# Kernel optimization log

Measured on AMD Instinct MI355X. Metric: run time of the kernel, lower is better.

## Reference

```python
import jax, jax.numpy as jnp
import numpy as np

N, E = 50000, 1600000
D_IN, H, N_REL, D_OUT = 518, 256, 10, 128


def setup_inputs() -> dict:
    key = jax.random.key(0)
    ks = jax.random.split(key, 20)
    def lin(k, fan_in, fan_out):
        bound = 1.0 / np.sqrt(fan_in)
        kw, kb = jax.random.split(k)
        W = jax.random.uniform(kw, (fan_in, fan_out), jnp.float32, -bound, bound)
        b = jax.random.uniform(kb, (fan_out,), jnp.float32, -bound, bound)
        return W, b
    x = jax.random.normal(ks[0], (N, D_IN), jnp.float32)
    edge_index = jax.random.randint(ks[1], (2, E), 0, N, jnp.int32)
    edge_attr = jax.random.randint(ks[2], (E,), 0, N_REL, jnp.int32)
    W_enc1, b_enc1 = lin(ks[3], D_IN, H)
    W_enc2, b_enc2 = lin(ks[4], H, H)
    emb_table = jax.random.normal(ks[5], (N_REL, H // 4), jnp.float32)
    W_g1, b_g1 = lin(ks[6], H, H)
    W_g2, b_g2 = lin(ks[7], H, H)
    W_g3, b_g3 = lin(ks[8], H, H)
    W_h1, b_h1 = lin(ks[9], H, H // 2)
    W_h2, b_h2 = lin(ks[10], H // 2, D_OUT)
    return dict(x=x, edge_index=edge_index, edge_attr=edge_attr,
                W_enc1=W_enc1, b_enc1=b_enc1, W_enc2=W_enc2, b_enc2=b_enc2,
                emb_table=emb_table,
                W_g1=W_g1, b_g1=b_g1, W_g2=W_g2, b_g2=b_g2, W_g3=W_g3, b_g3=b_g3,
                W_h1=W_h1, b_h1=b_h1, W_h2=W_h2, b_h2=b_h2)


def reference(x, edge_index, edge_attr,
              W_enc1, b_enc1, W_enc2, b_enc2, emb_table,
              W_g1, b_g1, W_g2, b_g2, W_g3, b_g3,
              W_h1, b_h1, W_h2, b_h2):
    src, dst = edge_index[0], edge_index[1]
    n = x.shape[0]
    # GCN symmetric normalization with self-loops: deg = 1 + in-degree
    deg = 1.0 + jax.ops.segment_sum(jnp.ones_like(src, jnp.float32), dst, num_segments=n)
    dis = deg ** -0.5                       # [N]
    norm_e = dis[src] * dis[dst]            # [E] edge norm
    self_norm = (dis * dis)[:, None]        # [N,1] self-loop norm

    def gcn(h, W, b):
        hw = h @ W                           # [N,H]
        agg = jax.ops.segment_sum(hw[src] * norm_e[:, None], dst, num_segments=n)
        return agg + hw * self_norm + b

    # node encoder (dropout is identity in eval)
    h = jax.nn.relu(x @ W_enc1 + b_enc1) @ W_enc2 + b_enc2
    _edge_emb = emb_table[edge_attr]         # computed as in original (unused downstream)
    h = jax.nn.relu(gcn(h, W_g1, b_g1))
    h = jax.nn.relu(gcn(h, W_g2, b_g2))
    h = jax.nn.relu(gcn(h, W_g3, b_g3))
    graph_repr = jnp.mean(h, axis=0, keepdims=True)   # batch=None path -> [1,H]
    out = jax.nn.relu(graph_repr @ W_h1 + b_h1) @ W_h2 + b_h2
    return out
```

## Files before the change

### kernel.cpp

```cpp
#include <hip/hip_runtime.h>

#define D_IN 518
#define HD 256
#define KP1 544
#define AGG_CAP 4096

typedef __attribute__((ext_vector_type(8))) short bf16x8;
typedef __attribute__((ext_vector_type(4))) float f32x4;
typedef __attribute__((ext_vector_type(4), aligned(4))) float float4u;
typedef __attribute__((ext_vector_type(4))) unsigned int uint4v;
typedef __attribute__((ext_vector_type(8))) unsigned short ushort8v;

__device__ __forceinline__ float bf2f(unsigned short u) {
  union { unsigned int i; float f; } v; v.i = ((unsigned int)u) << 16; return v.f;
}
__device__ __forceinline__ unsigned short f2bf(float f) {
  union { float f; unsigned int i; } v; v.f = f;
  unsigned int r = (v.i + 0x7FFFu + ((v.i >> 16) & 1u)) >> 16;
  return (unsigned short)r;
}

__global__ void k_canary(float* __restrict__ out, float code) {
  out[threadIdx.x] = code;
}


__global__ void k_hist(const int* __restrict__ dst, int E, int* __restrict__ cnt) {
  int e = (blockIdx.x * blockDim.x + threadIdx.x) * 4;
  if (e < E) {
    int4 d = *(const int4*)(dst + e);
    atomicAdd(&cnt[d.x], 1);
    atomicAdd(&cnt[d.y], 1);
    atomicAdd(&cnt[d.z], 1);
    atomicAdd(&cnt[d.w], 1);
  }
}

__global__ void k_blocksum(const int* __restrict__ cnt, int n, int* __restrict__ bsum) {
  __shared__ int red[256];
  const int t = threadIdx.x;
  int v = blockIdx.x * 256 + t;
  red[t] = (v < n) ? cnt[v] : 0;
  __syncthreads();
  for (int d = 128; d > 0; d >>= 1) {
    if (t < d) red[t] += red[t + d];
    __syncthreads();
  }
  if (t == 0) bsum[blockIdx.x] = red[0];
}

__global__ void k_scan_mid(const int* __restrict__ bsum, int nb, int* __restrict__ bex) {
  __shared__ int s[256];
  const int t = threadIdx.x;
  int x = (t < nb) ? bsum[t] : 0;
  s[t] = x;
  __syncthreads();
  for (int d = 1; d < 256; d <<= 1) {
    int v = (t >= d) ? s[t - d] : 0;
    __syncthreads();
    s[t] += v;
    __syncthreads();
  }
  if (t < nb) bex[t] = s[t] - x;
}

__global__ void k_off(const int* __restrict__ cnt, int n, const int* __restrict__ bex,
                      int* __restrict__ off, int* __restrict__ cursor,
                      float* __restrict__ dis) {
  __shared__ int s[256];
  const int t = threadIdx.x;
  const int v = blockIdx.x * 256 + t;
  int c = (v < n) ? cnt[v] : 0;
  s[t] = c;
  __syncthreads();
  for (int d = 1; d < 256; d <<= 1) {
    int x = (t >= d) ? s[t - d] : 0;
    __syncthreads();
    s[t] += x;
    __syncthreads();
  }
  if (v < n) {
    int incl = bex[blockIdx.x] + s[t];
    off[v + 1] = incl;
    cursor[v] = incl - c;
    dis[v] = 1.0f / sqrtf(1.0f + (float)c);
    if (v == 0) off[0] = 0;
  }
}

__global__ void k_fill_range(const int* __restrict__ src, const int* __restrict__ dst, int E,
                             int* __restrict__ cursor, unsigned short* __restrict__ csr,
                             int lo, int hi) {
  int e = (blockIdx.x * blockDim.x + threadIdx.x) * 4;
  if (e < E) {
    int4 d = *(const int4*)(dst + e);
    int4 s = *(const int4*)(src + e);
    if (d.x >= lo && d.x < hi) csr[atomicAdd(&cursor[d.x], 1)] = (unsigned short)s.x;
    if (d.y >= lo && d.y < hi) csr[atomicAdd(&cursor[d.y], 1)] = (unsigned short)s.y;
    if (d.z >= lo && d.z < hi) csr[atomicAdd(&cursor[d.z], 1)] = (unsigned short)s.z;
    if (d.w >= lo && d.w < hi) csr[atomicAdd(&cursor[d.w], 1)] = (unsigned short)s.w;
  }
}


__global__ void k_wt(const float* __restrict__ W, int K, int N, int Kp,
                     unsigned short* __restrict__ Wt) {
  int idx = blockIdx.x * blockDim.x + threadIdx.x;
  if (idx < N * Kp) {
    int n = idx / Kp, k = idx - n * Kp;
    Wt[idx] = (k < K) ? f2bf(W[k * N + n]) : (unsigned short)0;
  }
}

__global__ void k_wt4(const float* __restrict__ a, const float* __restrict__ b,
                      const float* __restrict__ c, const float* __restrict__ d,
                      unsigned short* __restrict__ oa, unsigned short* __restrict__ ob,
                      unsigned short* __restrict__ oc, unsigned short* __restrict__ od) {
  const float* W = (blockIdx.y == 0) ? a : (blockIdx.y == 1) ? b : (blockIdx.y == 2) ? c : d;
  unsigned short* O = (blockIdx.y == 0) ? oa : (blockIdx.y == 1) ? ob : (blockIdx.y == 2) ? oc : od;
  int idx = blockIdx.x * blockDim.x + threadIdx.x;
  int n = idx >> 8, k = idx & 255;
  O[idx] = f2bf(W[k * HD + n]);
}


__global__ __launch_bounds__(256, 2)
void k_gemm_bt(const unsigned short* __restrict__ A, int lda, int M, int K,
               const unsigned short* __restrict__ Bt, int ldb,
               const float* __restrict__ bias, const float* __restrict__ rowscale,
               int do_relu,
               unsigned short* __restrict__ C, int ldc, int sliced, int Mp) {
  const int bid = blockIdx.x;
  const int pair = (bid >> 4) * 8 + (bid & 7);
  const int mtiles = (M + 127) >> 7;
  if (pair >= mtiles) return;
  const int m0 = pair << 7;
  const int n0 = ((bid >> 3) & 1) << 7;

  __shared__ unsigned short As[128 * 40];
  __shared__ unsigned short Bs[128 * 40];
  const int tid = threadIdx.x;
  const int lane = tid & 63, wave = tid >> 6;
  const int q = lane >> 4, l15 = lane & 15;
  const int wm = (wave & 1) * 64, wn = (wave >> 1) * 64;

  f32x4 acc[4][4];
#pragma unroll
  for (int i = 0; i < 4; i++)
#pragma unroll
    for (int j = 0; j < 4; j++) acc[i][j] = f32x4{0.f, 0.f, 0.f, 0.f};

  const int r0 = tid >> 2, kb = tid & 3;
  int gmA0 = m0 + r0;       if (gmA0 >= M) gmA0 = M - 1;
  int gmA1 = m0 + r0 + 64;  if (gmA1 >= M) gmA1 = M - 1;
  const unsigned short* Arow0 = A + (size_t)gmA0 * lda;
  const unsigned short* Arow1 = A + (size_t)gmA1 * lda;
  const unsigned short* Brow0 = Bt + (size_t)(n0 + r0) * ldb;
  const unsigned short* Brow1 = Bt + (size_t)(n0 + r0 + 64) * ldb;
  unsigned short* lA0 = &As[r0 * 40 + kb * 8];
  unsigned short* lA1 = &As[(r0 + 64) * 40 + kb * 8];
  unsigned short* lB0 = &Bs[r0 * 40 + kb * 8];
  unsigned short* lB1 = &Bs[(r0 + 64) * 40 + kb * 8];

  for (int k0 = 0; k0 < K; k0 += 32) {
    __syncthreads();
    const int gk = k0 + kb * 8;
    *(bf16x8*)lA0 = *(const bf16x8*)(Arow0 + gk);
    *(bf16x8*)lA1 = *(const bf16x8*)(Arow1 + gk);
    *(bf16x8*)lB0 = *(const bf16x8*)(Brow0 + gk);
    *(bf16x8*)lB1 = *(const bf16x8*)(Brow1 + gk);
    __syncthreads();

    bf16x8 af[4], bfr[4];
#pragma unroll
    for (int i = 0; i < 4; i++)
      af[i] = *(const bf16x8*)(&As[(wm + i * 16 + l15) * 40 + q * 8]);
#pragma unroll
    for (int j = 0; j < 4; j++)
      bfr[j] = *(const bf16x8*)(&Bs[(wn + j * 16 + l15) * 40 + q * 8]);
#pragma unroll
    for (int i = 0; i < 4; i++)
#pragma unroll
      for (int j = 0; j < 4; j++)
        acc[i][j] = __builtin_amdgcn_mfma_f32_16x16x32_bf16(af[i], bfr[j], acc[i][j], 0, 0, 0);
  }

  const size_t Mp32 = (size_t)Mp * 32;
#pragma unroll
  for (int j = 0; j < 4; j++) {
    const int col = n0 + wn + j * 16 + l15;
    const float bv = bias ? bias[col] : 0.f;
    unsigned short* cb = sliced ? (C + (size_t)(col >> 5) * Mp32 + (col & 31))
                                : (C + col);
    const int rstr = sliced ? 32 : ldc;
#pragma unroll
    for (int i = 0; i < 4; i++) {
#pragma unroll
      for (int rg = 0; rg < 4; rg++) {
        int gr = m0 + wm + i * 16 + q * 4 + rg;
        if (gr < M) {
          float v = acc[i][j][rg];
          if (rowscale) v *= rowscale[gr];
          v += bv;
          if (do_relu) v = fmaxf(v, 0.f);
          cb[(size_t)gr * rstr] = f2bf(v);
        }
      }
    }
  }
}


__global__ __launch_bounds__(256, 2)
void k_gemm_f32in(const float* __restrict__ A, int lda, int M, int Kreal, int Kloop,
                  const unsigned short* __restrict__ Bt, int ldb,
                  const float* __restrict__ bias, int do_relu,
                  unsigned short* __restrict__ C, int ldc) {
  const int bid = blockIdx.x;
  const int pair = (bid >> 4) * 8 + (bid & 7);
  const int mtiles = (M + 127) >> 7;
  if (pair >= mtiles) return;
  const int m0 = pair << 7;
  const int n0 = ((bid >> 3) & 1) << 7;

  __shared__ unsigned short As[128 * 40];
  __shared__ unsigned short Bs[128 * 40];
  const int tid = threadIdx.x;
  const int lane = tid & 63, wave = tid >> 6;
  const int q = lane >> 4, l15 = lane & 15;
  const int wm = (wave & 1) * 64, wn = (wave >> 1) * 64;

  f32x4 acc[4][4];
#pragma unroll
  for (int i = 0; i < 4; i++)
#pragma unroll
    for (int j = 0; j < 4; j++) acc[i][j] = f32x4{0.f, 0.f, 0.f, 0.f};

  const int r0 = tid >> 2, kb = tid & 3;
  int gmA0 = m0 + r0;       if (gmA0 >= M) gmA0 = M - 1;
  int gmA1 = m0 + r0 + 64;  if (gmA1 >= M) gmA1 = M - 1;
  const float* Arow0 = A + (size_t)gmA0 * lda;
  const float* Arow1 = A + (size_t)gmA1 * lda;
  const unsigned short* Brow0 = Bt + (size_t)(n0 + r0) * ldb;
  const unsigned short* Brow1 = Bt + (size_t)(n0 + r0 + 64) * ldb;
  unsigned short* lA0 = &As[r0 * 40 + kb * 8];
  unsigned short* lA1 = &As[(r0 + 64) * 40 + kb * 8];
  unsigned short* lB0 = &Bs[r0 * 40 + kb * 8];
  unsigned short* lB1 = &Bs[(r0 + 64) * 40 + kb * 8];

  for (int k0 = 0; k0 < Kloop; k0 += 32) {
    __syncthreads();
    const int gk = k0 + kb * 8;
    if (gk + 8 <= Kreal) {
      float4u a0 = *(const float4u*)(Arow0 + gk);
      float4u a1 = *(const float4u*)(Arow0 + gk + 4);
      float4u b0 = *(const float4u*)(Arow1 + gk);
      float4u b1 = *(const float4u*)(Arow1 + gk + 4);
      bf16x8 t0, t1;
      t0[0] = (short)f2bf(a0.x); t0[1] = (short)f2bf(a0.y);
      t0[2] = (short)f2bf(a0.z); t0[3] = (short)f2bf(a0.w);
      t0[4] = (short)f2bf(a1.x); t0[5] = (short)f2bf(a1.y);
      t0[6] = (short)f2bf(a1.z); t0[7] = (short)f2bf(a1.w);
      t1[0] = (short)f2bf(b0.x); t1[1] = (short)f2bf(b0.y);
      t1[2] = (short)f2bf(b0.z); t1[3] = (short)f2bf(b0.w);
      t1[4] = (short)f2bf(b1.x); t1[5] = (short)f2bf(b1.y);
      t1[6] = (short)f2bf(b1.z); t1[7] = (short)f2bf(b1.w);
      *(bf16x8*)lA0 = t0;
      *(bf16x8*)lA1 = t1;
    } else {
      bf16x8 t0, t1;
#pragma unroll
      for (int t = 0; t < 8; t++) {
        int kk = gk + t;
        t0[t] = (short)((kk < Kreal) ? f2bf(Arow0[kk]) : (unsigned short)0);
        t1[t] = (short)((kk < Kreal) ? f2bf(Arow1[kk]) : (unsigned short)0);
      }
      *(bf16x8*)lA0 = t0;
      *(bf16x8*)lA1 = t1;
    }
    *(bf16x8*)lB0 = *(const bf16x8*)(Brow0 + gk);
    *(bf16x8*)lB1 = *(const bf16x8*)(Brow1 + gk);
    __syncthreads();

    bf16x8 af[4], bfr[4];
#pragma unroll
    for (int i = 0; i < 4; i++)
      af[i] = *(const bf16x8*)(&As[(wm + i * 16 + l15) * 40 + q * 8]);
#pragma unroll
    for (int j = 0; j < 4; j++)
      bfr[j] = *(const bf16x8*)(&Bs[(wn + j * 16 + l15) * 40 + q * 8]);
#pragma unroll
    for (int i = 0; i < 4; i++)
#pragma unroll
      for (int j = 0; j < 4; j++)
        acc[i][j] = __builtin_amdgcn_mfma_f32_16x16x32_bf16(af[i], bfr[j], acc[i][j], 0, 0, 0);
  }

#pragma unroll
  for (int j = 0; j < 4; j++) {
    const int col = n0 + wn + j * 16 + l15;
    const float bv = bias ? bias[col] : 0.f;
#pragma unroll
    for (int i = 0; i < 4; i++) {
#pragma unroll
      for (int rg = 0; rg < 4; rg++) {
        int gr = m0 + wm + i * 16 + q * 4 + rg;
        if (gr < M) {
          float v = acc[i][j][rg] + bv;
          if (do_relu) v = fmaxf(v, 0.f);
          C[(size_t)gr * ldc + col] = f2bf(v);
        }
      }
    }
  }
}


__global__ __launch_bounds__(256, 6)
void k_agg_sl(const unsigned short* __restrict__ hw_sl, int Mp,
              const int* __restrict__ off, const unsigned short* __restrict__ csr,
              const float* __restrict__ dis, const float* __restrict__ bias,
              unsigned short* __restrict__ hout, int n) {
  __shared__ unsigned short lidx[AGG_CAP];
  __shared__ int lodd[65];
  const int slice = blockIdx.x & 7;
  const int chunk = blockIdx.x >> 3;
  const int tid = threadIdx.x;
  const int wave = tid >> 6, lane = tid & 63;
  const int eg = lane >> 2, cl = lane & 3;
  const unsigned short* panel = hw_sl + (size_t)slice * ((size_t)Mp * 32) + (cl << 3);

  const int base = chunk << 6;
  int nv = n - base; if (nv > 64) nv = 64;
  if (tid <= nv) lodd[tid] = off[base + tid];
  __syncthreads();
  const int blk_e0 = lodd[0];
  const int tot = lodd[nv] - blk_e0;
  const bool use_lds = (tot <= AGG_CAP);
  if (use_lds) {
    for (int i = tid; i < tot; i += 256) lidx[i] = csr[blk_e0 + i];
  }
  __syncthreads();

  const int lv = (wave << 4) + eg;
  if (lv >= nv) return;
  const int v = base + lv;
  const int e0 = lodd[lv];
  const int cnt = lodd[lv + 1] - e0;
  float a[8];
#pragma unroll
  for (int k = 0; k < 8; ++k) a[k] = 0.f;

  if (use_lds) {
    const int le = e0 - blk_e0;
    int it = 0;
    for (; it + 8 <= cnt; it += 8) {
      int s[8];
#pragma unroll
      for (int p = 0; p < 8; ++p) s[p] = (int)lidx[le + it + p];
      uint4v d[8];
#pragma unroll
      for (int p = 0; p < 8; ++p)
        d[p] = *(const uint4v*)(panel + ((size_t)s[p] << 5));
#pragma unroll
      for (int p = 0; p < 8; ++p) {
#pragma unroll
        for (int w = 0; w < 4; ++w) {
          a[2 * w]     += __uint_as_float(d[p][w] << 16);
          a[2 * w + 1] += __uint_as_float(d[p][w] & 0xFFFF0000u);
        }
      }
    }
    for (; it < cnt; ++it) {
      int sp = (int)lidx[le + it];
      uint4v d = *(const uint4v*)(panel + ((size_t)sp << 5));
#pragma unroll
      for (int w = 0; w < 4; ++w) {
        a[2 * w]     += __uint_as_float(d[w] << 16);
        a[2 * w + 1] += __uint_as_float(d[w] & 0xFFFF0000u);
      }
    }
  } else {
    const unsigned short* me = csr + e0;
    int it = 0;
    for (; it + 8 <= cnt; it += 8) {
      int s[8];
#pragma unroll
      for (int p = 0; p < 8; ++p) s[p] = (int)me[it + p];
      uint4v d[8];
#pragma unroll
      for (int p = 0; p < 8; ++p)
        d[p] = *(const uint4v*)(panel + ((size_t)s[p] << 5));
#pragma unroll
      for (int p = 0; p < 8; ++p) {
#pragma unroll
        for (int w = 0; w < 4; ++w) {
          a[2 * w]     += __uint_as_float(d[p][w] << 16);
          a[2 * w + 1] += __uint_as_float(d[p][w] & 0xFFFF0000u);
        }
      }
    }
    for (; it < cnt; ++it) {
      int sp = (int)me[it];
      uint4v d = *(const uint4v*)(panel + ((size_t)sp << 5));
#pragma unroll
      for (int w = 0; w < 4; ++w) {
        a[2 * w]     += __uint_as_float(d[w] << 16);
        a[2 * w + 1] += __uint_as_float(d[w] & 0xFFFF0000u);
      }
    }
  }

  {
    uint4v ds_ = *(const uint4v*)(panel + ((size_t)v << 5));
#pragma unroll
    for (int w = 0; w < 4; ++w) {
      a[2 * w]     += __uint_as_float(ds_[w] << 16);
      a[2 * w + 1] += __uint_as_float(ds_[w] & 0xFFFF0000u);
    }
  }
  const float dv = dis[v];
  const float4u bv0 = *(const float4u*)(bias + (slice << 5) + (cl << 3));
  const float4u bv1 = *(const float4u*)(bias + (slice << 5) + (cl << 3) + 4);
  ushort8v o;
  o[0] = f2bf(fmaxf(dv * a[0] + bv0.x, 0.f));
  o[1] = f2bf(fmaxf(dv * a[1] + bv0.y, 0.f));
  o[2] = f2bf(fmaxf(dv * a[2] + bv0.z, 0.f));
  o[3] = f2bf(fmaxf(dv * a[3] + bv0.w, 0.f));
  o[4] = f2bf(fmaxf(dv * a[4] + bv1.x, 0.f));
  o[5] = f2bf(fmaxf(dv * a[5] + bv1.y, 0.f));
  o[6] = f2bf(fmaxf(dv * a[6] + bv1.z, 0.f));
  o[7] = f2bf(fmaxf(dv * a[7] + bv1.w, 0.f));
  *(ushort8v*)(hout + ((size_t)v << 8) + (slice << 5) + (cl << 3)) = o;
}


__global__ void k_colsum(const unsigned short* __restrict__ h, int n, float* __restrict__ gsum) {
  const int t = threadIdx.x;
  const int per = (n + gridDim.x - 1) / gridDim.x;
  const int rs = blockIdx.x * per;
  int re = rs + per; if (re > n) re = n;
  float s = 0.f;
  for (int r = rs; r < re; ++r) s += bf2f(h[(size_t)r * HD + t]);
  atomicAdd(&gsum[t], s);
}

__global__ void k_head(const float* __restrict__ gsum, float invN,
                       const float* __restrict__ Wh1, const float* __restrict__ bh1,
                       const float* __restrict__ Wh2, const float* __restrict__ bh2,
                       float* __restrict__ out) {
  __shared__ float g[256];
  __shared__ float t1[128];
  const int t = threadIdx.x;
  g[t] = gsum[t] * invN;
  g[t + 128] = gsum[t + 128] * invN;
  __syncthreads();
  float s = bh1[t];
  for (int k = 0; k < 256; ++k) s += g[k] * Wh1[k * 128 + t];
  t1[t] = fmaxf(s, 0.f);
  __syncthreads();
  float o = bh2[t];
  for (int j = 0; j < 128; ++j) o += t1[j] * Wh2[j * 128 + t];
  out[t] = o;
}


extern "C" void kernel_launch(void* const* d_in, const int* in_sizes, int n_in,
                              void* d_out, int out_size, void* d_ws, size_t ws_size,
                              hipStream_t stream) {
  float* outp = (float*)d_out;

  const float* x   = (const float*)d_in[0];
  const int* ei    = (const int*)d_in[1];
  const float* W1  = (const float*)d_in[3];
  const float* b1  = (const float*)d_in[4];
  const float* W2  = (const float*)d_in[5];
  const float* b2  = (const float*)d_in[6];
  const float* Wg1 = (const float*)d_in[8];
  const float* bg1 = (const float*)d_in[9];
  const float* Wg2 = (const float*)d_in[10];
  const float* bg2 = (const float*)d_in[11];
  const float* Wg3 = (const float*)d_in[12];
  const float* bg3 = (const float*)d_in[13];
  const float* Wh1 = (const float*)d_in[14];
  const float* bh1 = (const float*)d_in[15];
  const float* Wh2 = (const float*)d_in[16];
  const float* bh2 = (const float*)d_in[17];

  const int n = 50000;
  const int E = 1600000;
  const int nb = (n + 255) / 256;
  const int Mp = (n + 127) & ~127;
  const int* srcp = ei;
  const int* dstp = ei + E;

  char* p = (char*)d_ws;
  size_t used = 0;
  auto alloc = [&](size_t bytes) -> char* {
    char* r = p; size_t rb = (bytes + 255) & ~((size_t)255);
    p += rb; used += rb; return r;
  };
  int*   cnt    = (int*)alloc((size_t)n * 4);
  int*   off    = (int*)alloc((size_t)(n + 1) * 4);
  int*   cursor = (int*)alloc((size_t)n * 4);
  float* dis    = (float*)alloc((size_t)n * 4);
  int*   bsum   = (int*)alloc((size_t)nb * 4);
  int*   bex    = (int*)alloc((size_t)nb * 4);
  float* gsum   = (float*)alloc(256 * 4);
  unsigned short* csr = (unsigned short*)alloc((size_t)E * 2);
  unsigned short* W1t  = (unsigned short*)alloc((size_t)HD * KP1 * 2);
  unsigned short* W2t  = (unsigned short*)alloc((size_t)HD * HD * 2);
  unsigned short* Wg1t = (unsigned short*)alloc((size_t)HD * HD * 2);
  unsigned short* Wg2t = (unsigned short*)alloc((size_t)HD * HD * 2);
  unsigned short* Wg3t = (unsigned short*)alloc((size_t)HD * HD * 2);
  unsigned short* P    = (unsigned short*)alloc((size_t)Mp * HD * 2);
  unsigned short* Q    = (unsigned short*)alloc((size_t)n * HD * 2);

  if (used > ws_size) { k_canary<<<1, 128, 0, stream>>>(outp, 90000.0f); return; }

  hipMemsetAsync(cnt, 0, (size_t)n * 4, stream);
  hipMemsetAsync(gsum, 0, 256 * 4, stream);

  k_hist<<<(E / 4 + 255) / 256, 256, 0, stream>>>(dstp, E, cnt);
  k_blocksum<<<nb, 256, 0, stream>>>(cnt, n, bsum);
  k_scan_mid<<<1, 256, 0, stream>>>(bsum, nb, bex);
  k_off<<<nb, 256, 0, stream>>>(cnt, n, bex, off, cursor, dis);
  {
    const int NPASS = 2, span = (n + NPASS - 1) / NPASS;
    for (int i = 0; i < NPASS; ++i) {
      int lo = i * span, hi = lo + span; if (hi > n) hi = n;
      k_fill_range<<<(E / 4 + 255) / 256, 256, 0, stream>>>(srcp, dstp, E, cursor, csr, lo, hi);
    }
  }

  k_wt<<<(HD * KP1 + 255) / 256, 256, 0, stream>>>(W1, D_IN, HD, KP1, W1t);
  {
    dim3 g4(HD * HD / 256, 4);
    k_wt4<<<g4, 256, 0, stream>>>(W2, Wg1, Wg2, Wg3, W2t, Wg1t, Wg2t, Wg3t);
  }

  const int mtiles = (n + 127) / 128;
  const int gblocks = ((mtiles + 7) / 8) * 16;
  const int agrid = ((n + 63) / 64) * 8;

  k_gemm_f32in<<<gblocks, 256, 0, stream>>>(x, D_IN, n, D_IN, KP1, W1t, KP1, b1, 1, P, HD);
  k_gemm_bt<<<gblocks, 256, 0, stream>>>(P, HD, n, HD, W2t, HD, b2, nullptr, 0, Q, HD, 0, Mp);
  k_gemm_bt<<<gblocks, 256, 0, stream>>>(Q, HD, n, HD, Wg1t, HD, nullptr, dis, 0, P, HD, 1, Mp);
  k_agg_sl<<<agrid, 256, 0, stream>>>(P, Mp, off, csr, dis, bg1, Q, n);
  k_gemm_bt<<<gblocks, 256, 0, stream>>>(Q, HD, n, HD, Wg2t, HD, nullptr, dis, 0, P, HD, 1, Mp);
  k_agg_sl<<<agrid, 256, 0, stream>>>(P, Mp, off, csr, dis, bg2, Q, n);
  k_gemm_bt<<<gblocks, 256, 0, stream>>>(Q, HD, n, HD, Wg3t, HD, nullptr, dis, 0, P, HD, 1, Mp);
  k_agg_sl<<<agrid, 256, 0, stream>>>(P, Mp, off, csr, dis, bg3, Q, n);

  k_colsum<<<256, 256, 0, stream>>>(Q, n, gsum);
  k_head<<<1, 128, 0, stream>>>(gsum, 1.0f / (float)n, Wh1, bh1, Wh2, bh2, outp);
}
```

Before: 778.2 us.

## Use direct global-to-LDS loads in GEMM tiles and prefetch fp32 A

Both GEMM kernels now stage bf16 tiles with the global_load_lds builtin, which writes 16 bytes per lane straight into LDS without passing through registers. To fit that instruction's contiguous per-wave layout, the LDS row pitch drops from 40 to 32 elements. The fp32-input encoder GEMM also loads the next A slice into registers before the current slice's MFMAs, so the load latency overlaps compute. Removing the padding may bring back LDS bank conflicts on the fragment reads.

```diff
diff --git a/kernel.cpp b/kernel.cpp
--- a/kernel.cpp
+++ b/kernel.cpp
@@ -18,6 +18,12 @@
   union { float f; unsigned int i; } v; v.f = f;
   unsigned int r = (v.i + 0x7FFFu + ((v.i >> 16) & 1u)) >> 16;
   return (unsigned short)r;
+}
+
+__device__ __forceinline__ void gl_lds16(const unsigned short* g, unsigned short* l) {
+  __builtin_amdgcn_global_load_lds(
+      (const __attribute__((address_space(1))) unsigned int*)g,
+      (__attribute__((address_space(3))) unsigned int*)l, 16, 0, 0);
 }
 
 __global__ void k_canary(float* __restrict__ out, float code) {
@@ -137,8 +143,8 @@
   const int m0 = pair << 7;
   const int n0 = ((bid >> 3) & 1) << 7;
 
-  __shared__ unsigned short As[128 * 40];
-  __shared__ unsigned short Bs[128 * 40];
+  __shared__ unsigned short As[128 * 32];
+  __shared__ unsigned short Bs[128 * 32];
   const int tid = threadIdx.x;
   const int lane = tid & 63, wave = tid >> 6;
   const int q = lane >> 4, l15 = lane & 15;
@@ -150,34 +156,34 @@
 #pragma unroll
     for (int j = 0; j < 4; j++) acc[i][j] = f32x4{0.f, 0.f, 0.f, 0.f};
 
-  const int r0 = tid >> 2, kb = tid & 3;
-  int gmA0 = m0 + r0;       if (gmA0 >= M) gmA0 = M - 1;
-  int gmA1 = m0 + r0 + 64;  if (gmA1 >= M) gmA1 = M - 1;
-  const unsigned short* Arow0 = A + (size_t)gmA0 * lda;
-  const unsigned short* Arow1 = A + (size_t)gmA1 * lda;
-  const unsigned short* Brow0 = Bt + (size_t)(n0 + r0) * ldb;
-  const unsigned short* Brow1 = Bt + (size_t)(n0 + r0 + 64) * ldb;
-  unsigned short* lA0 = &As[r0 * 40 + kb * 8];
-  unsigned short* lA1 = &As[(r0 + 64) * 40 + kb * 8];
-  unsigned short* lB0 = &Bs[r0 * 40 + kb * 8];
-  unsigned short* lB1 = &Bs[(r0 + 64) * 40 + kb * 8];
+  const int rA = wave * 32 + (lane >> 2);
+  const int kc = (lane & 3) * 8;
+  int gA0 = m0 + rA;        if (gA0 >= M) gA0 = M - 1;
+  int gA1 = m0 + rA + 16;   if (gA1 >= M) gA1 = M - 1;
+  const unsigned short* pa0 = A + (size_t)gA0 * lda + kc;
+  const unsigned short* pa1 = A + (size_t)gA1 * lda + kc;
+  const unsigned short* pb0 = Bt + (size_t)(n0 + rA) * ldb + kc;
+  const unsigned short* pb1 = Bt + (size_t)(n0 + rA + 16) * ldb + kc;
+  unsigned short* la0 = &As[(wave * 32) * 32];
+  unsigned short* la1 = &As[(wave * 32 + 16) * 32];
+  unsigned short* lb0 = &Bs[(wave * 32) * 32];
+  unsigned short* lb1 = &Bs[(wave * 32 + 16) * 32];
 
   for (int k0 = 0; k0 < K; k0 += 32) {
     __syncthreads();
-    const int gk = k0 + kb * 8;
-    *(bf16x8*)lA0 = *(const bf16x8*)(Arow0 + gk);
-    *(bf16x8*)lA1 = *(const bf16x8*)(Arow1 + gk);
-    *(bf16x8*)lB0 = *(const bf16x8*)(Brow0 + gk);
-    *(bf16x8*)lB1 = *(const bf16x8*)(Brow1 + gk);
+    gl_lds16(pa0 + k0, la0);
+    gl_lds16(pa1 + k0, la1);
+    gl_lds16(pb0 + k0, lb0);
+    gl_lds16(pb1 + k0, lb1);
     __syncthreads();
 
     bf16x8 af[4], bfr[4];
 #pragma unroll
     for (int i = 0; i < 4; i++)
-      af[i] = *(const bf16x8*)(&As[(wm + i * 16 + l15) * 40 + q * 8]);
+      af[i] = *(const bf16x8*)(&As[(wm + i * 16 + l15) * 32 + q * 8]);
 #pragma unroll
     for (int j = 0; j < 4; j++)
-      bfr[j] = *(const bf16x8*)(&Bs[(wn + j * 16 + l15) * 40 + q * 8]);
+      bfr[j] = *(const bf16x8*)(&Bs[(wn + j * 16 + l15) * 32 + q * 8]);
 #pragma unroll
     for (int i = 0; i < 4; i++)
 #pragma unroll
@@ -223,8 +229,8 @@
   const int m0 = pair << 7;
   const int n0 = ((bid >> 3) & 1) << 7;
 
-  __shared__ unsigned short As[128 * 40];
-  __shared__ unsigned short Bs[128 * 40];
+  __shared__ unsigned short As[128 * 32];
+  __shared__ unsigned short Bs[128 * 32];
   const int tid = threadIdx.x;
   const int lane = tid & 63, wave = tid >> 6;
   const int q = lane >> 4, l15 = lane & 15;
@@ -241,54 +247,62 @@
   int gmA1 = m0 + r0 + 64;  if (gmA1 >= M) gmA1 = M - 1;
   const float* Arow0 = A + (size_t)gmA0 * lda;
   const float* Arow1 = A + (size_t)gmA1 * lda;
-  const unsigned short* Brow0 = Bt + (size_t)(n0 + r0) * ldb;
-  const unsigned short* Brow1 = Bt + (size_t)(n0 + r0 + 64) * ldb;
-  unsigned short* lA0 = &As[r0 * 40 + kb * 8];
-  unsigned short* lA1 = &As[(r0 + 64) * 40 + kb * 8];
-  unsigned short* lB0 = &Bs[r0 * 40 + kb * 8];
-  unsigned short* lB1 = &Bs[(r0 + 64) * 40 + kb * 8];
-
-  for (int k0 = 0; k0 < Kloop; k0 += 32) {
-    __syncthreads();
-    const int gk = k0 + kb * 8;
+  unsigned short* lA0 = &As[r0 * 32 + kb * 8];
+  unsigned short* lA1 = &As[(r0 + 64) * 32 + kb * 8];
+
+  const int rB = wave * 32 + (lane >> 2);
+  const int kc = (lane & 3) * 8;
+  const unsigned short* pb0 = Bt + (size_t)(n0 + rB) * ldb + kc;
+  const unsigned short* pb1 = Bt + (size_t)(n0 + rB + 16) * ldb + kc;
+  unsigned short* lb0 = &Bs[(wave * 32) * 32];
+  unsigned short* lb1 = &Bs[(wave * 32 + 16) * 32];
+
+  float a8[8], b8[8];
+  auto load_a = [&](int k0n) {
+    const int gk = k0n + kb * 8;
     if (gk + 8 <= Kreal) {
-      float4u a0 = *(const float4u*)(Arow0 + gk);
-      float4u a1 = *(const float4u*)(Arow0 + gk + 4);
-      float4u b0 = *(const float4u*)(Arow1 + gk);
-      float4u b1 = *(const float4u*)(Arow1 + gk + 4);
-      bf16x8 t0, t1;
-      t0[0] = (short)f2bf(a0.x); t0[1] = (short)f2bf(a0.y);
-      t0[2] = (short)f2bf(a0.z); t0[3] = (short)f2bf(a0.w);
-      t0[4] = (short)f2bf(a1.x); t0[5] = (short)f2bf(a1.y);
-      t0[6] = (short)f2bf(a1.z); t0[7] = (short)f2bf(a1.w);
-      t1[0] = (short)f2bf(b0.x); t1[1] = (short)f2bf(b0.y);
-      t1[2] = (short)f2bf(b0.z); t1[3] = (short)f2bf(b0.w);
-      t1[4] = (short)f2bf(b1.x); t1[5] = (short)f2bf(b1.y);
-      t1[6] = (short)f2bf(b1.z); t1[7] = (short)f2bf(b1.w);
-      *(bf16x8*)lA0 = t0;
-      *(bf16x8*)lA1 = t1;
+      float4u v0 = *(const float4u*)(Arow0 + gk);
+      float4u v1 = *(const float4u*)(Arow0 + gk + 4);
+      float4u w0 = *(const float4u*)(Arow1 + gk);
+      float4u w1 = *(const float4u*)(Arow1 + gk + 4);
+      a8[0] = v0.x; a8[1] = v0.y; a8[2] = v0.z; a8[3] = v0.w;
+      a8[4] = v1.x; a8[5] = v1.y; a8[6] = v1.z; a8[7] = v1.w;
+      b8[0] = w0.x; b8[1] = w0.y; b8[2] = w0.z; b8[3] = w0.w;
+      b8[4] = w1.x; b8[5] = w1.y; b8[6] = w1.z; b8[7] = w1.w;
     } else {
-      bf16x8 t0, t1;
 #pragma unroll
       for (int t = 0; t < 8; t++) {
         int kk = gk + t;
-        t0[t] = (short)((kk < Kreal) ? f2bf(Arow0[kk]) : (unsigned short)0);
-        t1[t] = (short)((kk < Kreal) ? f2bf(Arow1[kk]) : (unsigned short)0);
-      }
-      *(bf16x8*)lA0 = t0;
-      *(bf16x8*)lA1 = t1;
-    }
-    *(bf16x8*)lB0 = *(const bf16x8*)(Brow0 + gk);
-    *(bf16x8*)lB1 = *(const bf16x8*)(Brow1 + gk);
-    __syncthreads();
+        a8[t] = (kk < Kreal) ? Arow0[kk] : 0.f;
+        b8[t] = (kk < Kreal) ? Arow1[kk] : 0.f;
+      }
+    }
+  };
+  load_a(0);
+
+  for (int k0 = 0; k0 < Kloop; k0 += 32) {
+    __syncthreads();
+    bf16x8 t0, t1;
+#pragma unroll
+    for (int t = 0; t < 8; t++) {
+      t0[t] = (short)f2bf(a8[t]);
+      t1[t] = (short)f2bf(b8[t]);
+    }
+    *(bf16x8*)lA0 = t0;
+    *(bf16x8*)lA1 = t1;
+    gl_lds16(pb0 + k0, lb0);
+    gl_lds16(pb1 + k0, lb1);
+    __syncthreads();
+
+    if (k0 + 32 < Kloop) load_a(k0 + 32);
 
     bf16x8 af[4], bfr[4];
 #pragma unroll
     for (int i = 0; i < 4; i++)
-      af[i] = *(const bf16x8*)(&As[(wm + i * 16 + l15) * 40 + q * 8]);
+      af[i] = *(const bf16x8*)(&As[(wm + i * 16 + l15) * 32 + q * 8]);
 #pragma unroll
     for (int j = 0; j < 4; j++)
-      bfr[j] = *(const bf16x8*)(&Bs[(wn + j * 16 + l15) * 40 + q * 8]);
+      bfr[j] = *(const bf16x8*)(&Bs[(wn + j * 16 + l15) * 32 + q * 8]);
 #pragma unroll
     for (int i = 0; i < 4; i++)
 #pragma unroll
```

Result: no change. 775.2 us (-0.4%).
